# Optimization experiments

Hardware: AMD Instinct MI355X
Metric: run time of the kernel (lower is better)

## Reference

```python
import jax, jax.numpy as jnp
import numpy as np

N_NODES = 100000
N_EDGES = 1600000
IN_DIM = 512
HID_DIM = 64
N_CLASSES = 10
N_GRAPHS = 64


def setup_inputs() -> dict:
    key = jax.random.key(0)
    ks = jax.random.split(key, 8)
    x = jax.random.normal(ks[0], (N_NODES, IN_DIM), dtype=jnp.float32)
    edge_src = jax.random.randint(ks[1], (N_EDGES,), 0, N_NODES)
    edge_dst = jax.random.randint(ks[2], (N_EDGES,), 0, N_NODES)
    node2graph = jnp.sort(jax.random.randint(ks[3], (N_NODES,), 0, N_GRAPHS))
    W1 = jax.random.normal(ks[4], (IN_DIM, HID_DIM), dtype=jnp.float32) * (1.0 / np.sqrt(IN_DIM))
    b1 = jnp.zeros((HID_DIM,), dtype=jnp.float32)
    W2 = jax.random.normal(ks[5], (HID_DIM, N_CLASSES), dtype=jnp.float32) * (1.0 / np.sqrt(HID_DIM))
    b2 = jnp.zeros((N_CLASSES,), dtype=jnp.float32)
    return {"x": x, "edge_src": edge_src, "edge_dst": edge_dst,
            "node2graph": node2graph, "n_graphs": N_GRAPHS,
            "W1": W1, "b1": b1, "W2": W2, "b2": b2}


def reference(x, edge_src, edge_dst, node2graph, n_graphs, W1, b1, W2, b2):
    n = x.shape[0]
    ones_e = jnp.ones(edge_src.shape[0], dtype=x.dtype)
    # DGL GraphConv norm='both': src scaled by out-deg^-1/2, dst by in-deg^-1/2 (degrees clamped to 1)
    out_deg = jax.ops.segment_sum(ones_e, edge_src, num_segments=n)
    in_deg = jax.ops.segment_sum(ones_e, edge_dst, num_segments=n)
    src_norm = jax.lax.rsqrt(jnp.maximum(out_deg, 1.0))  # [N]
    dst_norm = jax.lax.rsqrt(jnp.maximum(in_deg, 1.0))   # [N]

    def graph_conv(h, W, b):
        h = (h * src_norm[:, None]) @ W                       # [N, out]
        agg = jax.ops.segment_sum(h[edge_src], edge_dst, num_segments=n)  # SpMM
        return agg * dst_norm[:, None] + b

    h = jax.nn.relu(graph_conv(x, W1, b1))
    h = graph_conv(h, W2, b2)
    # dgl.mean_nodes: per-graph mean over nodes
    counts = jax.ops.segment_sum(jnp.ones(n, dtype=x.dtype), node2graph, num_segments=n_graphs)
    sums = jax.ops.segment_sum(h, node2graph, num_segments=n_graphs)
    return sums / jnp.maximum(counts, 1.0)[:, None]
```

## Files before the change

kernel.cpp:

```cpp
#include <hip/hip_runtime.h>

#define NN 100000
#define NE 1600000
#define NG 64
#define BPB  50
#define NBUK 2000
#define NBUK2 2048
#define ECAP 1152
#define GPART 256
#define NSLICE 8
#define SLB (GPART/NSLICE)
#define PREPB 128
#define ZEROB 3
#define GSTB ((NN+255)/256)

using bf16x8 = __attribute__((ext_vector_type(8))) short;
using f32x4  = __attribute__((ext_vector_type(4))) float;

__device__ inline unsigned short f2bf(float f){
    union { float f; unsigned u; } v; v.f = f;
    unsigned r = (v.u + 0x7FFFu + ((v.u >> 16) & 1u)) >> 16;
    return (unsigned short)r;
}

__device__ inline bf16x8 cvt8(float4 a, float4 b){
    union { unsigned u[4]; bf16x8 v; } r;
    asm("v_cvt_pk_bf16_f32 %0, %1, %2" : "=v"(r.u[0]) : "v"(a.x), "v"(a.y));
    asm("v_cvt_pk_bf16_f32 %0, %1, %2" : "=v"(r.u[1]) : "v"(a.z), "v"(a.w));
    asm("v_cvt_pk_bf16_f32 %0, %1, %2" : "=v"(r.u[2]) : "v"(b.x), "v"(b.y));
    asm("v_cvt_pk_bf16_f32 %0, %1, %2" : "=v"(r.u[3]) : "v"(b.z), "v"(b.w));
    return r.v;
}

__global__ __launch_bounds__(256) void k_start(const int* __restrict__ src, const int* __restrict__ dst,
                                               int* __restrict__ cntD, int* __restrict__ cntS, int E,
                                               const float* __restrict__ W1, short* __restrict__ Wb,
                                               float* __restrict__ pooled,
                                               unsigned short* __restrict__ hb, float* __restrict__ h2,
                                               const int* __restrict__ n2g, int* __restrict__ gstart, int N){
    __shared__ int hD[NBUK2], hS[NBUK2];
    int bid = blockIdx.x;
    int tid = threadIdx.x;
    if (bid < GPART){
        for (int i=tid; i<NBUK2; i+=256){ hD[i]=0; hS[i]=0; }
        __syncthreads();
        int EV = E >> 2;
        int chunkV = (EV + GPART - 1)/GPART;
        int sV = bid*chunkV, eV = min(EV, sV+chunkV);
        for (int v = sV + tid; v < eV; v += 256){
            int4 s4 = ((const int4*)src)[v];
            int4 d4 = ((const int4*)dst)[v];
            atomicAdd(&hS[s4.x/BPB], 1); atomicAdd(&hS[s4.y/BPB], 1);
            atomicAdd(&hS[s4.z/BPB], 1); atomicAdd(&hS[s4.w/BPB], 1);
            atomicAdd(&hD[d4.x/BPB], 1); atomicAdd(&hD[d4.y/BPB], 1);
            atomicAdd(&hD[d4.z/BPB], 1); atomicAdd(&hD[d4.w/BPB], 1);
        }
        __syncthreads();
        for (int i=tid; i<NBUK2; i+=256){
            cntD[bid*NBUK2 + i] = hD[i];
            cntS[bid*NBUK2 + i] = hS[i];
        }
    } else if (bid < GPART+PREPB){
        int i = (bid-GPART)*256 + tid;
        if (i < 512*64){
            int k = i >> 6, c = i & 63;
            int g = k >> 5, r = k & 31, s = r >> 3, j = r & 7;
            Wb[(((g*4+s)*64 + c) << 3) + j] = (short)f2bf(W1[i]);
        }
    } else if (bid < GPART+PREPB+ZEROB){
        int i = (bid-GPART-PREPB)*256 + tid;
        if (i < NG*10) pooled[i] = 0.f;
        else if (i < NG*10 + 64) hb[(size_t)N*64 + (i - NG*10)] = 0;
        else if (i < NG*10 + 64 + 16) h2[(size_t)N*16 + (i - NG*10 - 64)] = 0.f;
    } else {
        int n = (bid-GPART-PREPB-ZEROB)*256 + tid;
        if (n < N){
            int g  = n2g[n];
            int gp = (n == 0) ? -1 : n2g[n-1];
            if (gp != g){
                for (int gg = gp+1; gg <= g; ++gg) gstart[gg] = n;
            }
            if (n == N-1){
                for (int gg = g+1; gg <= NG; ++gg) gstart[gg] = N;
            }
        }
    }
}

__global__ __launch_bounds__(256) void k_scanCa(const int* __restrict__ cntD, const int* __restrict__ cntS,
                                                int* __restrict__ sliceD, int* __restrict__ sliceS){
    int id = blockIdx.x*256 + threadIdx.x;
    int t = id & (NBUK2-1);
    int s = id >> 11;
    int b0 = s*SLB;
    int sD=0, sS=0;
    for (int b=b0; b<b0+SLB; b++){ sD += cntD[b*NBUK2+t]; sS += cntS[b*NBUK2+t]; }
    sliceD[s*NBUK2+t] = sD;
    sliceS[s*NBUK2+t] = sS;
}

__global__ __launch_bounds__(1024) void k_scanB(const int* __restrict__ sliceD, const int* __restrict__ sliceS,
                                                int* __restrict__ bstartD, int* __restrict__ bstartS){
    __shared__ int sd[1024];
    int t = threadIdx.x;
    {
        int v0=0, v1=0;
        #pragma unroll
        for (int s=0;s<NSLICE;s++){ v0 += sliceD[s*NBUK2 + 2*t]; v1 += sliceD[s*NBUK2 + 2*t+1]; }
        sd[t] = v0+v1; __syncthreads();
        for (int off=1; off<1024; off<<=1){
            int tv = (t >= off) ? sd[t-off] : 0;
            __syncthreads();
            sd[t] += tv;
            __syncthreads();
        }
        int excl = sd[t] - v0 - v1;
        if (2*t   <= NBUK) bstartD[2*t]   = excl;
        if (2*t+1 <= NBUK) bstartD[2*t+1] = excl + v0;
        __syncthreads();
    }
    {
        int v0=0, v1=0;
        #pragma unroll
        for (int s=0;s<NSLICE;s++){ v0 += sliceS[s*NBUK2 + 2*t]; v1 += sliceS[s*NBUK2 + 2*t+1]; }
        sd[t] = v0+v1; __syncthreads();
        for (int off=1; off<1024; off<<=1){
            int tv = (t >= off) ? sd[t-off] : 0;
            __syncthreads();
            sd[t] += tv;
            __syncthreads();
        }
        int excl = sd[t] - v0 - v1;
        if (2*t   <= NBUK) bstartS[2*t]   = excl;
        if (2*t+1 <= NBUK) bstartS[2*t+1] = excl + v0;
    }
}

__global__ __launch_bounds__(256) void k_scanCb(int* __restrict__ cntD, int* __restrict__ cntS,
                                                const int* __restrict__ sliceD, const int* __restrict__ sliceS,
                                                const int* __restrict__ bstartD, const int* __restrict__ bstartS){
    int id = blockIdx.x*256 + threadIdx.x;
    int t = id & (NBUK2-1);
    int s = id >> 11;
    if (t >= NBUK) return;
    int rD = bstartD[t], rS = bstartS[t];
    for (int sp=0; sp<s; sp++){ rD += sliceD[sp*NBUK2+t]; rS += sliceS[sp*NBUK2+t]; }
    int b0 = s*SLB;
    for (int b=b0; b<b0+SLB; b++){
        int idx = b*NBUK2 + t;
        int o = cntD[idx]; cntD[idx] = rD; rD += o;
        o = cntS[idx];     cntS[idx] = rS; rS += o;
    }
}

__global__ __launch_bounds__(256) void k_scatter(const int* __restrict__ src, const int* __restrict__ dst,
                                                 const int* __restrict__ cntD, const int* __restrict__ cntS,
                                                 int* __restrict__ pairs, unsigned char* __restrict__ srcb, int E){
    __shared__ unsigned oD[NBUK2], oS[NBUK2];
    for (int i=threadIdx.x; i<NBUK2; i+=256){
        oD[i] = (unsigned)cntD[blockIdx.x*NBUK2 + i];
        oS[i] = (unsigned)cntS[blockIdx.x*NBUK2 + i];
    }
    __syncthreads();
    int EV = E >> 2;
    int chunkV = (EV + GPART - 1)/GPART;
    int sV = blockIdx.x*chunkV, eV = min(EV, sV+chunkV);
    for (int v = sV + threadIdx.x; v < eV; v += 256){
        int4 s4 = ((const int4*)src)[v];
        int4 d4 = ((const int4*)dst)[v];
        #pragma unroll
        for (int k=0;k<4;k++){
            int s = (k==0)?s4.x:(k==1)?s4.y:(k==2)?s4.z:s4.w;
            int d = (k==0)?d4.x:(k==1)?d4.y:(k==2)?d4.z:d4.w;
            int bk = d/BPB;
            unsigned pD = atomicAdd(&oD[bk], 1u);
            pairs[pD] = (s << 6) | (d - bk*BPB);
            int sb = s/BPB;
            unsigned pS = atomicAdd(&oS[sb], 1u);
            srcb[pS] = (unsigned char)(s - sb*BPB);
        }
    }
}

__global__ __launch_bounds__(256) void k_outdeg(const unsigned char* __restrict__ srcb,
                                                const int* __restrict__ bstartS,
                                                float* __restrict__ sn, int N){
    __shared__ int c[BPB];
    int b = blockIdx.x;
    if (threadIdx.x < BPB) c[threadIdx.x] = 0;
    __syncthreads();
    int s0 = bstartS[b], s1 = bstartS[b+1];
    for (int i = s0 + threadIdx.x; i < s1; i += 256)
        atomicAdd(&c[srcb[i]], 1);
    __syncthreads();
    int node = b*BPB + threadIdx.x;
    if (threadIdx.x < BPB && node < N)
        sn[node] = rsqrtf((float)max(c[threadIdx.x], 1));
}

__global__ __launch_bounds__(256) void k_gemm1(const float* __restrict__ x, const short* __restrict__ Wb,
                                               const float* __restrict__ sn, unsigned short* __restrict__ hb, int N){
    const int lane = threadIdx.x & 63;
    const int wid  = threadIdx.x >> 6;
    const int rowBase = blockIdx.x*128 + wid*32;
    const int mrow = lane & 15;
    const int s    = lane >> 4;

    int rowA = rowBase + mrow;
    int rowB = rowBase + 16 + mrow;
    int rcA = (rowA < N) ? rowA : (N-1);
    int rcB = (rowB < N) ? rowB : (N-1);

    const float4* __restrict__ xv = (const float4*)x;
    const bf16x8* __restrict__ wv = (const bf16x8*)Wb;
    const float4* xrA = xv + (size_t)rcA*128 + s*2;
    const float4* xrB = xv + (size_t)rcB*128 + s*2;

    f32x4 accA0 = {0,0,0,0}, accA1 = {0,0,0,0}, accA2 = {0,0,0,0}, accA3 = {0,0,0,0};
    f32x4 accB0 = {0,0,0,0}, accB1 = {0,0,0,0}, accB2 = {0,0,0,0}, accB3 = {0,0,0,0};

    #pragma unroll 2
    for (int g=0; g<16; g++){
        float4 a0 = xrA[g*8 + 0];
        float4 a1 = xrA[g*8 + 1];
        float4 c0 = xrB[g*8 + 0];
        float4 c1 = xrB[g*8 + 1];
        bf16x8 afA = cvt8(a0, a1);
        bf16x8 afB = cvt8(c0, c1);
        int bbase = (g*4 + s)*64 + mrow;
        bf16x8 b0 = wv[bbase     ];
        bf16x8 b1 = wv[bbase + 16];
        bf16x8 b2 = wv[bbase + 32];
        bf16x8 b3 = wv[bbase + 48];
        accA0 = __builtin_amdgcn_mfma_f32_16x16x32_bf16(afA, b0, accA0, 0, 0, 0);
        accA1 = __builtin_amdgcn_mfma_f32_16x16x32_bf16(afA, b1, accA1, 0, 0, 0);
        accA2 = __builtin_amdgcn_mfma_f32_16x16x32_bf16(afA, b2, accA2, 0, 0, 0);
        accA3 = __builtin_amdgcn_mfma_f32_16x16x32_bf16(afA, b3, accA3, 0, 0, 0);
        accB0 = __builtin_amdgcn_mfma_f32_16x16x32_bf16(afB, b0, accB0, 0, 0, 0);
        accB1 = __builtin_amdgcn_mfma_f32_16x16x32_bf16(afB, b1, accB1, 0, 0, 0);
        accB2 = __builtin_amdgcn_mfma_f32_16x16x32_bf16(afB, b2, accB2, 0, 0, 0);
        accB3 = __builtin_amdgcn_mfma_f32_16x16x32_bf16(afB, b3, accB3, 0, 0, 0);
    }

    #pragma unroll
    for (int q=0; q<4; q++){
        int rr = rowBase + s*4 + q;
        if (rr < N){
            float scale = sn[rr];
            unsigned short* hp = hb + ((size_t)rr<<6) + mrow;
            hp[ 0] = f2bf(accA0[q] * scale);
            hp[16] = f2bf(accA1[q] * scale);
            hp[32] = f2bf(accA2[q] * scale);
            hp[48] = f2bf(accA3[q] * scale);
        }
        int r2 = rowBase + 16 + s*4 + q;
        if (r2 < N){
            float scale = sn[r2];
            unsigned short* hp = hb + ((size_t)r2<<6) + mrow;
            hp[ 0] = f2bf(accB0[q] * scale);
            hp[16] = f2bf(accB1[q] * scale);
            hp[32] = f2bf(accB2[q] * scale);
            hp[48] = f2bf(accB3[q] * scale);
        }
    }
}

__global__ __launch_bounds__(256) void k_agg(const int* __restrict__ pairs, const int* __restrict__ bstartD,
                                             const unsigned short* __restrict__ hb,
                                             const float* __restrict__ sn, const float* __restrict__ b1,
                                             const float* __restrict__ W2,
                                             float* __restrict__ h2, int* __restrict__ gsrc,
                                             int* __restrict__ glh, int N){
    __shared__ int lsrc[ECAP];
    __shared__ int lcnt[BPB];
    __shared__ int lstart[BPB+1];
    __shared__ unsigned lofs[BPB];
    __shared__ __align__(16) float w2t[10][64];
    __shared__ float b1s[64];
    __shared__ __align__(16) float a1s[BPB][68];
    int tid = threadIdx.x;
    if (tid < BPB) lcnt[tid] = 0;
    if (tid < 64)  b1s[tid] = b1[tid];
    for (int i=tid; i<ECAP; i+=256) lsrc[i] = N;
    for (int i=tid; i<640; i+=256){ int c = i>>6, k = i&63; w2t[c][k] = W2[k*10 + c]; }
    __syncthreads();

    int b = blockIdx.x;
    int nodeBase = b*BPB;
    int eb = bstartD[b], ee = bstartD[b+1];
    int ne = ee - eb;

    for (int i = tid; i < ne; i += 256){
        int pr = pairs[eb + i];
        atomicAdd(&lcnt[pr & 63], 1);
    }
    __syncthreads();
    if (tid < 64){
        int mt = (tid < BPB) ? lcnt[tid] : 0;
        int v = (mt + 3) & ~3;
        int sI = v;
        for (int off=1; off<64; off<<=1){
            int t = __shfl_up(sI, off);
            if (tid >= off) sI += t;
        }
        if (tid < BPB){
            lstart[tid] = sI - v;
            lofs[tid]   = (unsigned)(sI - v);
            if (tid == BPB-1) lstart[BPB] = sI;
        }
    }
    __syncthreads();
    for (int i = tid; i < ne; i += 256){
        int pr = pairs[eb + i];
        unsigned pos = atomicAdd(&lofs[pr & 63], 1u);
        lsrc[pos < ECAP ? pos : ECAP-1] = pr >> 6;
    }
    __syncthreads();

    int ptot = lstart[BPB];
    for (int i = tid; i < ptot; i += 256) gsrc[b*ECAP + i] = lsrc[i];
    if (tid <= BPB){
        int mt = (tid < BPB) ? lcnt[tid] : 0;
        glh[b*64 + tid] = (lstart[tid] & 0xFFFF) | (mt << 16);
    }

    int lane = tid & 63, wid = tid >> 6;
    int q  = lane >> 4;
    int c4 = lane & 15;

    for (int nl = wid; nl < BPB; nl += 4){
        int node = nodeBase + nl;
        int s0 = lstart[nl];
        int m4 = lstart[nl+1] - s0;
        int mt = lcnt[nl];

        float a0=0.f, a1f=0.f, a2=0.f, a3=0.f;
        int j = 0;
        for (; j + 16 <= m4; j += 16){
            int sa = lsrc[s0 + j + q];
            int sb = lsrc[s0 + j + 4 + q];
            int sc = lsrc[s0 + j + 8 + q];
            int sd = lsrc[s0 + j + 12 + q];
            uint2 va = *(const uint2*)(hb + ((size_t)sa<<6) + (c4<<2));
            uint2 vb = *(const uint2*)(hb + ((size_t)sb<<6) + (c4<<2));
            uint2 vc = *(const uint2*)(hb + ((size_t)sc<<6) + (c4<<2));
            uint2 vd = *(const uint2*)(hb + ((size_t)sd<<6) + (c4<<2));
            a0  += __uint_as_float((va.x & 0xffffu) << 16) + __uint_as_float((vb.x & 0xffffu) << 16)
                 + __uint_as_float((vc.x & 0xffffu) << 16) + __uint_as_float((vd.x & 0xffffu) << 16);
            a1f += __uint_as_float(va.x & 0xffff0000u) + __uint_as_float(vb.x & 0xffff0000u)
                 + __uint_as_float(vc.x & 0xffff0000u) + __uint_as_float(vd.x & 0xffff0000u);
            a2  += __uint_as_float((va.y & 0xffffu) << 16) + __uint_as_float((vb.y & 0xffffu) << 16)
                 + __uint_as_float((vc.y & 0xffffu) << 16) + __uint_as_float((vd.y & 0xffffu) << 16);
            a3  += __uint_as_float(va.y & 0xffff0000u) + __uint_as_float(vb.y & 0xffff0000u)
                 + __uint_as_float(vc.y & 0xffff0000u) + __uint_as_float(vd.y & 0xffff0000u);
        }
        for (; j < m4; j += 4){
            int sa = lsrc[s0 + j + q];
            uint2 va = *(const uint2*)(hb + ((size_t)sa<<6) + (c4<<2));
            a0  += __uint_as_float((va.x & 0xffffu) << 16);
            a1f += __uint_as_float(va.x & 0xffff0000u);
            a2  += __uint_as_float((va.y & 0xffffu) << 16);
            a3  += __uint_as_float(va.y & 0xffff0000u);
        }
        a0  += __shfl_xor(a0, 16);  a0  += __shfl_xor(a0, 32);
        a1f += __shfl_xor(a1f, 16); a1f += __shfl_xor(a1f, 32);
        a2  += __shfl_xor(a2, 16);  a2  += __shfl_xor(a2, 32);
        a3  += __shfl_xor(a3, 16);  a3  += __shfl_xor(a3, 32);

        float dnv = rsqrtf((float)max(mt, 1));
        float snv = sn[node];
        float r0 = fmaxf(fmaf(a0,  dnv, b1s[(c4<<2)+0]), 0.f) * snv;
        float r1 = fmaxf(fmaf(a1f, dnv, b1s[(c4<<2)+1]), 0.f) * snv;
        float r2 = fmaxf(fmaf(a2,  dnv, b1s[(c4<<2)+2]), 0.f) * snv;
        float r3 = fmaxf(fmaf(a3,  dnv, b1s[(c4<<2)+3]), 0.f) * snv;
        if (q == 0){
            *(float4*)(&a1s[nl][c4<<2]) = make_float4(r0, r1, r2, r3);
        }
    }
    __syncthreads();

    for (int i = tid; i < BPB*10; i += 256){
        int nl = i / 10;
        int c  = i - nl*10;
        int node = nodeBase + nl;
        if (node < N){
            const float4* ap = (const float4*)(&a1s[nl][0]);
            const float4* wp = (const float4*)(&w2t[c][0]);
            float acc = 0.f;
            #pragma unroll
            for (int p=0;p<16;p++){
                float4 a = ap[p]; float4 w = wp[p];
                acc = fmaf(a.x, w.x, fmaf(a.y, w.y, fmaf(a.z, w.z, fmaf(a.w, w.w, acc))));
            }
            h2[(size_t)node*16 + c] = acc;
        }
    }
}

__global__ __launch_bounds__(256) void k_pool2(const int* __restrict__ gsrc, const int* __restrict__ glh,
                                               const float* __restrict__ h2, const int* __restrict__ n2g,
                                               float* __restrict__ pooled, int N){
    __shared__ float accS[NG*10];
    int tid = threadIdx.x;
    for (int i=tid; i<NG*10; i+=256) accS[i] = 0.f;
    __syncthreads();
    int b = blockIdx.x;
    int nodeBase = b*BPB;
    int lane = tid & 63, wid = tid >> 6;
    int e6 = lane/10, c = lane - e6*10;
    bool active = (lane < 60);

    for (int nl = wid; nl < BPB; nl += 4){
        int node = nodeBase + nl;
        int cur = glh[b*64 + nl];
        int nxt = glh[b*64 + nl + 1];
        int base = b*ECAP + (cur & 0xFFFF);
        int m4   = (nxt & 0xFFFF) - (cur & 0xFFFF);
        int mt   = cur >> 16;
        float acc = 0.f;
        for (int j = 0; j < m4; j += 6){
            int idx = j + e6;
            int idxc = (idx < m4) ? idx : (m4-1);
            int srcn = gsrc[base + idxc];
            float v = h2[(size_t)srcn*16 + c];
            if (active && idx < m4) acc += v;
        }
        float t0 = __shfl(acc, lane+30); if (lane < 30) acc += t0;
        float t1 = __shfl(acc, lane+10);
        float t2 = __shfl(acc, lane+20);
        if (lane < 10){
            acc += t1 + t2;
            float dnv = rsqrtf((float)max(mt, 1));
            int g = n2g[node];
            atomicAdd(&accS[g*10 + lane], dnv*acc);
        }
    }
    __syncthreads();
    int g0 = n2g[nodeBase], g1 = n2g[nodeBase + BPB - 1];
    int lo = g0*10, hi = g1*10 + 10;
    for (int i = lo + tid; i < hi; i += 256)
        atomicAdd(&pooled[i], accS[i]);
}

__global__ void k_out(const float* __restrict__ pooled, const int* __restrict__ gstart,
                      const float* __restrict__ b2, float* __restrict__ out){
    int i = blockIdx.x*blockDim.x + threadIdx.x;
    if (i < NG*10){
        int g = i/10, c = i - g*10;
        float cnt = (float)max(gstart[g+1] - gstart[g], 1);
        out[i] = pooled[i]/cnt + b2[c];
    }
}

extern "C" void kernel_launch(void* const* d_in, const int* in_sizes, int n_in,
                              void* d_out, int out_size, void* d_ws, size_t ws_size,
                              hipStream_t stream) {
    const float* x    = (const float*)d_in[0];
    const int*   esrc = (const int*)d_in[1];
    const int*   edst = (const int*)d_in[2];
    const int*   n2g  = (const int*)d_in[3];
    const float* W1   = (const float*)d_in[5];
    const float* b1   = (const float*)d_in[6];
    const float* W2   = (const float*)d_in[7];
    const float* b2   = (const float*)d_in[8];
    float* out = (float*)d_out;
    const int N = in_sizes[3];
    const int E = in_sizes[1];

    char* ws = (char*)d_ws;
    size_t off = 0;
    auto alloc = [&](size_t bytes) -> void* {
        void* p = ws + off;
        off = (off + bytes + 255) & ~(size_t)255;
        return p;
    };
    float* pooled  = (float*)alloc(NG*10*4);
    int*   cntD    = (int*)alloc((size_t)GPART*NBUK2*4);
    int*   cntS    = (int*)alloc((size_t)GPART*NBUK2*4);
    int*   sliceD  = (int*)alloc((size_t)NSLICE*NBUK2*4);
    int*   sliceS  = (int*)alloc((size_t)NSLICE*NBUK2*4);
    int*   bstartD = (int*)alloc((NBUK+1)*4);
    int*   bstartS = (int*)alloc((NBUK+1)*4);
    int*   pairs   = (int*)alloc((size_t)E*4);
    unsigned char* srcb = (unsigned char*)alloc((size_t)E);
    int*   gsrc    = (int*)alloc((size_t)NBUK*ECAP*4);
    int*   glh     = (int*)alloc((size_t)NBUK*64*4);
    float* sn      = (float*)alloc((size_t)N*4);
    int*   gstart  = (int*)alloc((size_t)(NG+1)*4);
    short* Wb      = (short*)alloc((size_t)512*64*2);
    unsigned short* hb = (unsigned short*)alloc((size_t)(N+1)*64*2);
    float* h2      = (float*)alloc((size_t)(N+1)*16*4);

    k_start<<<dim3(GPART+PREPB+ZEROB+GSTB), dim3(256), 0, stream>>>(
        esrc, edst, cntD, cntS, E, W1, Wb, pooled, hb, h2, n2g, gstart, N);
    k_scanCa<<<dim3(64), dim3(256), 0, stream>>>(cntD, cntS, sliceD, sliceS);
    k_scanB<<<dim3(1), dim3(1024), 0, stream>>>(sliceD, sliceS, bstartD, bstartS);
    k_scanCb<<<dim3(64), dim3(256), 0, stream>>>(cntD, cntS, sliceD, sliceS, bstartD, bstartS);
    k_scatter<<<dim3(GPART), dim3(256), 0, stream>>>(esrc, edst, cntD, cntS, pairs, srcb, E);
    k_outdeg<<<dim3(NBUK), dim3(256), 0, stream>>>(srcb, bstartS, sn, N);

    k_gemm1<<<dim3((N+127)/128), dim3(256), 0, stream>>>(x, Wb, sn, hb, N);

    k_agg<<<dim3(NBUK), dim3(256), 0, stream>>>(pairs, bstartD, hb, sn, b1, W2, h2, gsrc, glh, N);
    k_pool2<<<dim3(NBUK), dim3(256), 0, stream>>>(gsrc, glh, h2, n2g, pooled, N);
    k_out<<<dim3(3), dim3(256), 0, stream>>>(pooled, gstart, b2, out);
}
```

Measured before the change: 218.6 us.

## Fuse scan, scatter and out-degree into one cooperative kernel; widen agg blocks

Merges five small preprocessing kernels (slice sums, bucket scan, scan apply, edge scatter, out-degree) into a single cooperative kernel separated by grid-wide syncs, so four kernel launch gaps disappear. The single-block scan is rewritten to use 256 threads with 8 elements each. Separately, the x loads in the first GEMM become nontemporal, and the aggregation kernel moves to 512-thread blocks with 8 warps per node loop. The grid syncs and the single-block scan phase leave most blocks idle, and the larger agg blocks may reduce occupancy.

```diff
diff --git a/kernel.cpp b/kernel.cpp
--- a/kernel.cpp
+++ b/kernel.cpp
@@ -1,4 +1,7 @@
 #include <hip/hip_runtime.h>
+#include <hip/hip_cooperative_groups.h>
+
+namespace cg = cooperative_groups;
 
 #define NN 100000
 #define NE 1600000
@@ -23,12 +26,12 @@
     return (unsigned short)r;
 }
 
-__device__ inline bf16x8 cvt8(float4 a, float4 b){
+__device__ inline bf16x8 cvt8(f32x4 a, f32x4 b){
     union { unsigned u[4]; bf16x8 v; } r;
-    asm("v_cvt_pk_bf16_f32 %0, %1, %2" : "=v"(r.u[0]) : "v"(a.x), "v"(a.y));
-    asm("v_cvt_pk_bf16_f32 %0, %1, %2" : "=v"(r.u[1]) : "v"(a.z), "v"(a.w));
-    asm("v_cvt_pk_bf16_f32 %0, %1, %2" : "=v"(r.u[2]) : "v"(b.x), "v"(b.y));
-    asm("v_cvt_pk_bf16_f32 %0, %1, %2" : "=v"(r.u[3]) : "v"(b.z), "v"(b.w));
+    asm("v_cvt_pk_bf16_f32 %0, %1, %2" : "=v"(r.u[0]) : "v"(a[0]), "v"(a[1]));
+    asm("v_cvt_pk_bf16_f32 %0, %1, %2" : "=v"(r.u[1]) : "v"(a[2]), "v"(a[3]));
+    asm("v_cvt_pk_bf16_f32 %0, %1, %2" : "=v"(r.u[2]) : "v"(b[0]), "v"(b[1]));
+    asm("v_cvt_pk_bf16_f32 %0, %1, %2" : "=v"(r.u[3]) : "v"(b[2]), "v"(b[3]));
     return r.v;
 }
 
@@ -87,115 +90,121 @@
     }
 }
 
-__global__ __launch_bounds__(256) void k_scanCa(const int* __restrict__ cntD, const int* __restrict__ cntS,
-                                                int* __restrict__ sliceD, int* __restrict__ sliceS){
-    int id = blockIdx.x*256 + threadIdx.x;
-    int t = id & (NBUK2-1);
-    int s = id >> 11;
-    int b0 = s*SLB;
-    int sD=0, sS=0;
-    for (int b=b0; b<b0+SLB; b++){ sD += cntD[b*NBUK2+t]; sS += cntS[b*NBUK2+t]; }
-    sliceD[s*NBUK2+t] = sD;
-    sliceS[s*NBUK2+t] = sS;
-}
-
-__global__ __launch_bounds__(1024) void k_scanB(const int* __restrict__ sliceD, const int* __restrict__ sliceS,
-                                                int* __restrict__ bstartD, int* __restrict__ bstartS){
-    __shared__ int sd[1024];
-    int t = threadIdx.x;
+__global__ __launch_bounds__(256) void k_mid(int* __restrict__ cntD, int* __restrict__ cntS,
+                                             int* __restrict__ sliceD, int* __restrict__ sliceS,
+                                             int* __restrict__ bstartD, int* __restrict__ bstartS,
+                                             const int* __restrict__ src, const int* __restrict__ dst,
+                                             int* __restrict__ pairs, unsigned char* __restrict__ srcb,
+                                             float* __restrict__ sn, int E, int N){
+    cg::grid_group grid = cg::this_grid();
+    __shared__ int shm[NBUK2*2];
+    int bid = blockIdx.x;
+    int tid = threadIdx.x;
+
+    if (bid < 64){
+        int id = bid*256 + tid;
+        int t = id & (NBUK2-1);
+        int s = id >> 11;
+        int b0 = s*SLB;
+        int sD=0, sS=0;
+        for (int b=b0; b<b0+SLB; b++){ sD += cntD[b*NBUK2+t]; sS += cntS[b*NBUK2+t]; }
+        sliceD[s*NBUK2+t] = sD;
+        sliceS[s*NBUK2+t] = sS;
+    }
+    grid.sync();
+
+    if (bid == 0){
+        int vD[8], vS[8];
+        int LD=0, LS=0;
+        #pragma unroll
+        for (int k=0;k<8;k++){
+            int t = tid*8+k;
+            int d=0, s=0;
+            #pragma unroll
+            for (int sp=0;sp<NSLICE;sp++){ d += sliceD[sp*NBUK2+t]; s += sliceS[sp*NBUK2+t]; }
+            vD[k]=d; vS[k]=s; LD+=d; LS+=s;
+        }
+        shm[tid] = LD; __syncthreads();
+        for (int off=1; off<256; off<<=1){
+            int t2 = (tid>=off)? shm[tid-off]:0; __syncthreads();
+            shm[tid]+=t2; __syncthreads();
+        }
+        int baseD = shm[tid]-LD;
+        __syncthreads();
+        shm[tid] = LS; __syncthreads();
+        for (int off=1; off<256; off<<=1){
+            int t2=(tid>=off)? shm[tid-off]:0; __syncthreads();
+            shm[tid]+=t2; __syncthreads();
+        }
+        int baseS = shm[tid]-LS;
+        int rD=baseD, rS=baseS;
+        #pragma unroll
+        for (int k=0;k<8;k++){
+            int t = tid*8+k;
+            if (t<=NBUK){ bstartD[t]=rD; bstartS[t]=rS; }
+            rD+=vD[k]; rS+=vS[k];
+        }
+    }
+    grid.sync();
+
+    if (bid < 64){
+        int id = bid*256 + tid;
+        int t = id & (NBUK2-1);
+        int s = id >> 11;
+        if (t < NBUK){
+            int rD = bstartD[t], rS = bstartS[t];
+            for (int sp=0; sp<s; sp++){ rD += sliceD[sp*NBUK2+t]; rS += sliceS[sp*NBUK2+t]; }
+            int b0 = s*SLB;
+            for (int b=b0; b<b0+SLB; b++){
+                int idx = b*NBUK2 + t;
+                int o = cntD[idx]; cntD[idx] = rD; rD += o;
+                o = cntS[idx];     cntS[idx] = rS; rS += o;
+            }
+        }
+    }
+    grid.sync();
+
     {
-        int v0=0, v1=0;
-        #pragma unroll
-        for (int s=0;s<NSLICE;s++){ v0 += sliceD[s*NBUK2 + 2*t]; v1 += sliceD[s*NBUK2 + 2*t+1]; }
-        sd[t] = v0+v1; __syncthreads();
-        for (int off=1; off<1024; off<<=1){
-            int tv = (t >= off) ? sd[t-off] : 0;
-            __syncthreads();
-            sd[t] += tv;
-            __syncthreads();
-        }
-        int excl = sd[t] - v0 - v1;
-        if (2*t   <= NBUK) bstartD[2*t]   = excl;
-        if (2*t+1 <= NBUK) bstartD[2*t+1] = excl + v0;
-        __syncthreads();
-    }
-    {
-        int v0=0, v1=0;
-        #pragma unroll
-        for (int s=0;s<NSLICE;s++){ v0 += sliceS[s*NBUK2 + 2*t]; v1 += sliceS[s*NBUK2 + 2*t+1]; }
-        sd[t] = v0+v1; __syncthreads();
-        for (int off=1; off<1024; off<<=1){
-            int tv = (t >= off) ? sd[t-off] : 0;
-            __syncthreads();
-            sd[t] += tv;
-            __syncthreads();
-        }
-        int excl = sd[t] - v0 - v1;
-        if (2*t   <= NBUK) bstartS[2*t]   = excl;
-        if (2*t+1 <= NBUK) bstartS[2*t+1] = excl + v0;
-    }
-}
-
-__global__ __launch_bounds__(256) void k_scanCb(int* __restrict__ cntD, int* __restrict__ cntS,
-                                                const int* __restrict__ sliceD, const int* __restrict__ sliceS,
-                                                const int* __restrict__ bstartD, const int* __restrict__ bstartS){
-    int id = blockIdx.x*256 + threadIdx.x;
-    int t = id & (NBUK2-1);
-    int s = id >> 11;
-    if (t >= NBUK) return;
-    int rD = bstartD[t], rS = bstartS[t];
-    for (int sp=0; sp<s; sp++){ rD += sliceD[sp*NBUK2+t]; rS += sliceS[sp*NBUK2+t]; }
-    int b0 = s*SLB;
-    for (int b=b0; b<b0+SLB; b++){
-        int idx = b*NBUK2 + t;
-        int o = cntD[idx]; cntD[idx] = rD; rD += o;
-        o = cntS[idx];     cntS[idx] = rS; rS += o;
-    }
-}
-
-__global__ __launch_bounds__(256) void k_scatter(const int* __restrict__ src, const int* __restrict__ dst,
-                                                 const int* __restrict__ cntD, const int* __restrict__ cntS,
-                                                 int* __restrict__ pairs, unsigned char* __restrict__ srcb, int E){
-    __shared__ unsigned oD[NBUK2], oS[NBUK2];
-    for (int i=threadIdx.x; i<NBUK2; i+=256){
-        oD[i] = (unsigned)cntD[blockIdx.x*NBUK2 + i];
-        oS[i] = (unsigned)cntS[blockIdx.x*NBUK2 + i];
-    }
-    __syncthreads();
-    int EV = E >> 2;
-    int chunkV = (EV + GPART - 1)/GPART;
-    int sV = blockIdx.x*chunkV, eV = min(EV, sV+chunkV);
-    for (int v = sV + threadIdx.x; v < eV; v += 256){
-        int4 s4 = ((const int4*)src)[v];
-        int4 d4 = ((const int4*)dst)[v];
-        #pragma unroll
-        for (int k=0;k<4;k++){
-            int s = (k==0)?s4.x:(k==1)?s4.y:(k==2)?s4.z:s4.w;
-            int d = (k==0)?d4.x:(k==1)?d4.y:(k==2)?d4.z:d4.w;
-            int bk = d/BPB;
-            unsigned pD = atomicAdd(&oD[bk], 1u);
-            pairs[pD] = (s << 6) | (d - bk*BPB);
-            int sb = s/BPB;
-            unsigned pS = atomicAdd(&oS[sb], 1u);
-            srcb[pS] = (unsigned char)(s - sb*BPB);
-        }
-    }
-}
-
-__global__ __launch_bounds__(256) void k_outdeg(const unsigned char* __restrict__ srcb,
-                                                const int* __restrict__ bstartS,
-                                                float* __restrict__ sn, int N){
-    __shared__ int c[BPB];
-    int b = blockIdx.x;
-    if (threadIdx.x < BPB) c[threadIdx.x] = 0;
-    __syncthreads();
-    int s0 = bstartS[b], s1 = bstartS[b+1];
-    for (int i = s0 + threadIdx.x; i < s1; i += 256)
-        atomicAdd(&c[srcb[i]], 1);
-    __syncthreads();
-    int node = b*BPB + threadIdx.x;
-    if (threadIdx.x < BPB && node < N)
-        sn[node] = rsqrtf((float)max(c[threadIdx.x], 1));
+        int* oD = shm;
+        int* oS = shm + NBUK2;
+        for (int i=tid; i<NBUK2; i+=256){
+            oD[i] = cntD[bid*NBUK2 + i];
+            oS[i] = cntS[bid*NBUK2 + i];
+        }
+        __syncthreads();
+        int EV = E >> 2;
+        int chunkV = (EV + GPART - 1)/GPART;
+        int sV = bid*chunkV, eV = min(EV, sV+chunkV);
+        for (int v = sV + tid; v < eV; v += 256){
+            int4 s4 = ((const int4*)src)[v];
+            int4 d4 = ((const int4*)dst)[v];
+            #pragma unroll
+            for (int k=0;k<4;k++){
+                int s = (k==0)?s4.x:(k==1)?s4.y:(k==2)?s4.z:s4.w;
+                int d = (k==0)?d4.x:(k==1)?d4.y:(k==2)?d4.z:d4.w;
+                int bk = d/BPB;
+                int pD = atomicAdd(&oD[bk], 1);
+                pairs[pD] = (s << 6) | (d - bk*BPB);
+                int sb = s/BPB;
+                int pS = atomicAdd(&oS[sb], 1);
+                srcb[pS] = (unsigned char)(s - sb*BPB);
+            }
+        }
+    }
+    grid.sync();
+
+    for (int b = bid; b < NBUK; b += gridDim.x){
+        if (tid < BPB) shm[tid] = 0;
+        __syncthreads();
+        int s0 = bstartS[b], s1 = bstartS[b+1];
+        for (int i = s0 + tid; i < s1; i += 256)
+            atomicAdd(&shm[srcb[i]], 1);
+        __syncthreads();
+        int node = b*BPB + tid;
+        if (tid < BPB && node < N)
+            sn[node] = rsqrtf((float)max(shm[tid], 1));
+        __syncthreads();
+    }
 }
 
 __global__ __launch_bounds__(256) void k_gemm1(const float* __restrict__ x, const short* __restrict__ Wb,
@@ -211,20 +220,20 @@
     int rcA = (rowA < N) ? rowA : (N-1);
     int rcB = (rowB < N) ? rowB : (N-1);
 
-    const float4* __restrict__ xv = (const float4*)x;
+    const f32x4* __restrict__ xv = (const f32x4*)x;
     const bf16x8* __restrict__ wv = (const bf16x8*)Wb;
-    const float4* xrA = xv + (size_t)rcA*128 + s*2;
-    const float4* xrB = xv + (size_t)rcB*128 + s*2;
+    const f32x4* xrA = xv + (size_t)rcA*128 + s*2;
+    const f32x4* xrB = xv + (size_t)rcB*128 + s*2;
 
     f32x4 accA0 = {0,0,0,0}, accA1 = {0,0,0,0}, accA2 = {0,0,0,0}, accA3 = {0,0,0,0};
     f32x4 accB0 = {0,0,0,0}, accB1 = {0,0,0,0}, accB2 = {0,0,0,0}, accB3 = {0,0,0,0};
 
     #pragma unroll 2
     for (int g=0; g<16; g++){
-        float4 a0 = xrA[g*8 + 0];
-        float4 a1 = xrA[g*8 + 1];
-        float4 c0 = xrB[g*8 + 0];
-        float4 c1 = xrB[g*8 + 1];
+        f32x4 a0 = __builtin_nontemporal_load(xrA + g*8 + 0);
+        f32x4 a1 = __builtin_nontemporal_load(xrA + g*8 + 1);
+        f32x4 c0 = __builtin_nontemporal_load(xrB + g*8 + 0);
+        f32x4 c1 = __builtin_nontemporal_load(xrB + g*8 + 1);
         bf16x8 afA = cvt8(a0, a1);
         bf16x8 afB = cvt8(c0, c1);
         int bbase = (g*4 + s)*64 + mrow;
@@ -265,7 +274,7 @@
     }
 }
 
-__global__ __launch_bounds__(256) void k_agg(const int* __restrict__ pairs, const int* __restrict__ bstartD,
+__global__ __launch_bounds__(512) void k_agg(const int* __restrict__ pairs, const int* __restrict__ bstartD,
                                              const unsigned short* __restrict__ hb,
                                              const float* __restrict__ sn, const float* __restrict__ b1,
                                              const float* __restrict__ W2,
@@ -281,8 +290,8 @@
     int tid = threadIdx.x;
     if (tid < BPB) lcnt[tid] = 0;
     if (tid < 64)  b1s[tid] = b1[tid];
-    for (int i=tid; i<ECAP; i+=256) lsrc[i] = N;
-    for (int i=tid; i<640; i+=256){ int c = i>>6, k = i&63; w2t[c][k] = W2[k*10 + c]; }
+    for (int i=tid; i<ECAP; i+=512) lsrc[i] = N;
+    for (int i=tid; i<640; i+=512){ int c = i>>6, k = i&63; w2t[c][k] = W2[k*10 + c]; }
     __syncthreads();
 
     int b = blockIdx.x;
@@ -290,7 +299,7 @@
     int eb = bstartD[b], ee = bstartD[b+1];
     int ne = ee - eb;
 
-    for (int i = tid; i < ne; i += 256){
+    for (int i = tid; i < ne; i += 512){
         int pr = pairs[eb + i];
         atomicAdd(&lcnt[pr & 63], 1);
     }
@@ -310,7 +319,7 @@
         }
     }
     __syncthreads();
-    for (int i = tid; i < ne; i += 256){
+    for (int i = tid; i < ne; i += 512){
         int pr = pairs[eb + i];
         unsigned pos = atomicAdd(&lofs[pr & 63], 1u);
         lsrc[pos < ECAP ? pos : ECAP-1] = pr >> 6;
@@ -318,7 +327,7 @@
     __syncthreads();
 
     int ptot = lstart[BPB];
-    for (int i = tid; i < ptot; i += 256) gsrc[b*ECAP + i] = lsrc[i];
+    for (int i = tid; i < ptot; i += 512) gsrc[b*ECAP + i] = lsrc[i];
     if (tid <= BPB){
         int mt = (tid < BPB) ? lcnt[tid] : 0;
         glh[b*64 + tid] = (lstart[tid] & 0xFFFF) | (mt << 16);
@@ -328,7 +337,7 @@
     int q  = lane >> 4;
     int c4 = lane & 15;
 
-    for (int nl = wid; nl < BPB; nl += 4){
+    for (int nl = wid; nl < BPB; nl += 8){
         int node = nodeBase + nl;
         int s0 = lstart[nl];
         int m4 = lstart[nl+1] - s0;
@@ -379,7 +388,7 @@
     }
     __syncthreads();
 
-    for (int i = tid; i < BPB*10; i += 256){
+    for (int i = tid; i < BPB*10; i += 512){
         int nl = i / 10;
         int c  = i - nl*10;
         int node = nodeBase + nl;
@@ -464,8 +473,8 @@
     const float* W2   = (const float*)d_in[7];
     const float* b2   = (const float*)d_in[8];
     float* out = (float*)d_out;
-    const int N = in_sizes[3];
-    const int E = in_sizes[1];
+    int N = in_sizes[3];
+    int E = in_sizes[1];
 
     char* ws = (char*)d_ws;
     size_t off = 0;
@@ -493,15 +502,15 @@
 
     k_start<<<dim3(GPART+PREPB+ZEROB+GSTB), dim3(256), 0, stream>>>(
         esrc, edst, cntD, cntS, E, W1, Wb, pooled, hb, h2, n2g, gstart, N);
-    k_scanCa<<<dim3(64), dim3(256), 0, stream>>>(cntD, cntS, sliceD, sliceS);
-    k_scanB<<<dim3(1), dim3(1024), 0, stream>>>(sliceD, sliceS, bstartD, bstartS);
-    k_scanCb<<<dim3(64), dim3(256), 0, stream>>>(cntD, cntS, sliceD, sliceS, bstartD, bstartS);
-    k_scatter<<<dim3(GPART), dim3(256), 0, stream>>>(esrc, edst, cntD, cntS, pairs, srcb, E);
-    k_outdeg<<<dim3(NBUK), dim3(256), 0, stream>>>(srcb, bstartS, sn, N);
+
+    void* margs[] = {(void*)&cntD, (void*)&cntS, (void*)&sliceD, (void*)&sliceS,
+                     (void*)&bstartD, (void*)&bstartS, (void*)&esrc, (void*)&edst,
+                     (void*)&pairs, (void*)&srcb, (void*)&sn, (void*)&E, (void*)&N};
+    (void)hipLaunchCooperativeKernel((void*)k_mid, dim3(GPART), dim3(256), margs, 0, stream);
 
     k_gemm1<<<dim3((N+127)/128), dim3(256), 0, stream>>>(x, Wb, sn, hb, N);
 
-    k_agg<<<dim3(NBUK), dim3(256), 0, stream>>>(pairs, bstartD, hb, sn, b1, W2, h2, gsrc, glh, N);
+    k_agg<<<dim3(NBUK), dim3(512), 0, stream>>>(pairs, bstartD, hb, sn, b1, W2, h2, gsrc, glh, N);
     k_pool2<<<dim3(NBUK), dim3(256), 0, stream>>>(gsrc, glh, h2, n2g, pooled, N);
     k_out<<<dim3(3), dim3(256), 0, stream>>>(pooled, gstart, b2, out);
 }
```

Result: slower. 352.6 us (+61.3%).
